# Performance work log

Measured on AMD Instinct MI355X. Metric: run time of the kernel, lower is better.

Reference implementation:

```python
import jax, jax.numpy as jnp
import numpy as np

N_HEADS = 4
D_HEAD = 16
SCALE = D_HEAD ** 0.5  # NOTE: original multiplies by sqrt(d_head), faithful


def _mha(x, Wq, bq, Wk, bk, Wv, bv, Wo, bo):
    # x: (..., N, D) with D = N_HEADS * D_HEAD
    q = jnp.einsum('...nd,od->...no', x, Wq) + bq
    k = jnp.einsum('...nd,od->...no', x, Wk) + bk
    v = jnp.einsum('...nd,od->...no', x, Wv) + bv
    lead = x.shape[:-2]
    n = x.shape[-2]
    q = q.reshape(*lead, n, N_HEADS, D_HEAD)
    k = k.reshape(*lead, n, N_HEADS, D_HEAD)
    v = v.reshape(*lead, n, N_HEADS, D_HEAD)
    scores = jnp.einsum('...nhd,...mhd->...hnm', q, k) * SCALE
    attn = jax.nn.softmax(scores, axis=-1)
    o = jnp.einsum('...hnm,...mhd->...nhd', attn, v).reshape(*lead, n, N_HEADS * D_HEAD)
    return jnp.einsum('...nd,od->...no', o, Wo) + bo


def setup_inputs() -> dict:
    key = jax.random.key(0)
    ks = jax.random.split(key, 20)
    b, n, d, dhf, G, C = 16, 16384, 64, 64, 256, 64
    s = 0.05
    inp = {
        'x': jax.random.normal(ks[0], (b, n, d), dtype=jnp.float32),
        'partitions': jax.random.permutation(ks[1], n).reshape(G, C).astype(jnp.int64),
    }
    names = ['q_intra', 'k_intra', 'v_intra', 'o_intra',
             'q_inter', 'k_inter', 'v_inter', 'o_inter']
    for i, nm in enumerate(names):
        d_in = d if nm.endswith('intra') and nm[0] != 'o' else dhf
        inp['W' + nm] = jax.random.normal(ks[2 + 2 * i], (dhf, d_in), dtype=jnp.float32) * s
        inp['b' + nm] = jax.random.normal(ks[3 + 2 * i], (dhf,), dtype=jnp.float32) * s
    return inp


def reference(x, partitions,
              Wq_intra, bq_intra, Wk_intra, bk_intra, Wv_intra, bv_intra, Wo_intra, bo_intra,
              Wq_inter, bq_inter, Wk_inter, bk_inter, Wv_inter, bv_inter, Wo_inter, bo_inter):
    b = x.shape[0]
    G, C = partitions.shape
    dhf = Wq_intra.shape[0]
    # gather nodes into groups: (b, G, C, d)
    xg = x[:, partitions, :]
    # intra-group attention, vectorized over (b, G)
    intra = _mha(xg, Wq_intra, bq_intra, Wk_intra, bk_intra,
                 Wv_intra, bv_intra, Wo_intra, bo_intra)  # (b, G, C, dhf)
    # MaxPool1d(kernel=dhf) over token axis with C == dhf -> max over tokens
    pooled = jnp.max(intra, axis=2)  # (b, G, dhf)
    inter = _mha(pooled, Wq_inter, bq_inter, Wk_inter, bk_inter,
                 Wv_inter, bv_inter, Wo_inter, bo_inter)  # (b, G, dhf)
    # broadcast-add inter-group features to every token in the group
    out = intra + inter[:, :, None, :]  # (b, G, C, dhf)
    flat = out.reshape(b, G * C, dhf)
    inv = jnp.argsort(partitions.reshape(-1))  # restore original node order
    return flat[:, inv, :]
```

## Files before the change

### kernel.cpp

```cpp
#include <hip/hip_runtime.h>
#include <hip/hip_bf16.h>

#define NTOK 16384
#define NG   256
#define NB   16

typedef float  f32x4   __attribute__((ext_vector_type(4)));
typedef short  short8v __attribute__((ext_vector_type(8)));
typedef short  short4v __attribute__((ext_vector_type(4)));

#define MFMA_BF16(a, b, c) __builtin_amdgcn_mfma_f32_16x16x32_bf16((a), (b), (c), 0, 0, 0)

#define QSCALE 5.770780163555856f

__device__ __forceinline__ short f2bf(float f) {
    union { float f; unsigned u; } x; x.f = f;
    unsigned r = (x.u + 0x7FFF + ((x.u >> 16) & 1)) >> 16;
    return (short)r;
}
__device__ __forceinline__ short bft(float f) {
    union { float f; unsigned u; } x; x.f = f;
    return (short)(x.u >> 16);
}
__device__ __forceinline__ float bf2f(short s) {
    union { float f; unsigned u; } x;
    x.u = ((unsigned)(unsigned short)s) << 16;
    return x.f;
}
__device__ __forceinline__ unsigned pk_cvt(float a, float b) {
#if __has_builtin(__builtin_amdgcn_cvt_pk_bf16_f32)
    auto r = __builtin_amdgcn_cvt_pk_bf16_f32(a, b);
    unsigned u; __builtin_memcpy(&u, &r, 4); return u;
#else
    union { float f; unsigned u; } xa, xb; xa.f = a; xb.f = b;
    const unsigned ua = xa.u + (0x7FFFu + ((xa.u >> 16) & 1));
    const unsigned ub = xb.u + (0x7FFFu + ((xb.u >> 16) & 1));
    return __builtin_amdgcn_perm(ub, ua, 0x07060302u);
#endif
}

__global__ void k_setup(const int* __restrict__ raw, int* __restrict__ part,
                        const float* __restrict__ Wq, const float* __restrict__ Wk,
                        const float* __restrict__ Wv, const float* __restrict__ Wo,
                        const float* __restrict__ Wqe, const float* __restrict__ Wke,
                        const float* __restrict__ Wve, const float* __restrict__ Woe,
                        short8v* __restrict__ wf)
{
    const int gid = blockIdx.x * 256 + threadIdx.x;
    if (gid < 16384) {
        const bool is64 = (raw[1] == 0 && raw[3] == 0 && raw[5] == 0);
        part[gid] = is64 ? raw[2 * gid] : raw[gid];
        return;
    }
    const int p = gid - 16384;
    if (p >= 5632) return;
    if (p < 3584) {
        const int v    = p >> 9;
        const int rem  = p & 511;
        const int tau  = rem >> 6;
        const int lane = rem & 63;
        const int jt = tau >> 1, kt = tau & 1;
        const int o  = jt * 16 + (lane & 15);
        const int d0 = kt * 32 + (lane >> 4) * 8;
        const float* W = (v < 2) ? Wq : (v < 4) ? Wk : (v < 6) ? Wv : Wo;
        const bool lo = (v & 1) && (v < 6);
        short8v r8;
#pragma unroll
        for (int i = 0; i < 8; ++i) {
            const float f = W[o * 64 + d0 + i];
            const short hh = f2bf(f);
            r8[i] = lo ? f2bf(f - bf2f(hh)) : hh;
        }
        wf[p] = r8;
    } else {
        const int g2   = p - 3584;
        const int v    = g2 >> 9;
        const int rem  = g2 & 511;
        const int tau  = rem >> 6;
        const int lane = rem & 63;
        const int jt = tau >> 1, kt = tau & 1;
        const int o  = jt * 16 + (lane & 15);
        const int d0 = kt * 32 + (lane >> 4) * 8;
        const float* W = (v == 0) ? Wqe : (v == 1) ? Wke : (v == 2) ? Wve : Woe;
        short8v r8;
#pragma unroll
        for (int i = 0; i < 8; ++i) r8[i] = f2bf(W[o * 64 + d0 + i]);
        wf[p] = r8;
    }
}

__global__ __launch_bounds__(256, 4) void k_intra(
    const float* __restrict__ x, const int* __restrict__ part,
    const short8v* __restrict__ wf,
    const float* __restrict__ bq, const float* __restrict__ bk,
    const float* __restrict__ bv, const float* __restrict__ bo,
    float* __restrict__ out, float* __restrict__ pooled,
    unsigned short* __restrict__ intra_g, const int use_g)
{
    __shared__ __align__(16) short S[20480];

    short* const xh = S;
    short* const kk = S + 4096;
    short* const ql = S + 8192;
    short* const qh = S + 12288;
    short* const vT = S + 16384;

    const int t  = threadIdx.x;
    const int g  = blockIdx.x;
    const int bb = blockIdx.y;
    const int l  = t & 63;
    const int w  = t >> 6;
    const int quad = l >> 4;
    const int col  = l & 15;

    for (int j = t; j < 512; j += 256) {
        const int row = j >> 3, c8 = j & 7;
        const int tok = part[g * 64 + row];
        const float* px = x + ((size_t)bb * NTOK + tok) * 64 + c8 * 8;
        const float4 f0 = ((const float4*)px)[0];
        const float4 f1 = ((const float4*)px)[1];
        uint4 pk;
        pk.x = pk_cvt(f0.x, f0.y);
        pk.y = pk_cvt(f0.z, f0.w);
        pk.z = pk_cvt(f1.x, f1.y);
        pk.w = pk_cvt(f1.z, f1.w);
        *(uint4*)&xh[row * 64 + ((c8 ^ (row & 7)) << 3)] = pk;
    }
    __syncthreads();

    {
        const float bqv = bq[w * 16 + col];
        const float bkv = bk[w * 16 + col];
        const float bvv = bv[w * 16 + col];
        short8v bqh[2], bql2[2], bkh[2], bkl[2], bvh[2], bvl[2];
#pragma unroll
        for (int kt = 0; kt < 2; ++kt) {
            const int tau = w * 2 + kt;
            bqh[kt]  = wf[(0 * 8 + tau) * 64 + l];
            bql2[kt] = wf[(1 * 8 + tau) * 64 + l];
            bkh[kt]  = wf[(2 * 8 + tau) * 64 + l];
            bkl[kt]  = wf[(3 * 8 + tau) * 64 + l];
            bvh[kt]  = wf[(4 * 8 + tau) * 64 + l];
            bvl[kt]  = wf[(5 * 8 + tau) * 64 + l];
        }
        for (int mt = 0; mt < 4; ++mt) {
            short8v axh[2];
#pragma unroll
            for (int kt = 0; kt < 2; ++kt) {
                const int row = mt * 16 + col;
                axh[kt] = *(const short8v*)&xh[row * 64 + (((kt * 4 + quad) ^ (row & 7)) << 3)];
            }
            f32x4 aq = {0.f, 0.f, 0.f, 0.f};
            f32x4 ak = {0.f, 0.f, 0.f, 0.f};
            f32x4 av = {0.f, 0.f, 0.f, 0.f};
#pragma unroll
            for (int kt = 0; kt < 2; ++kt) {
                aq = MFMA_BF16(axh[kt], bqh[kt],  aq);
                aq = MFMA_BF16(axh[kt], bql2[kt], aq);
                ak = MFMA_BF16(axh[kt], bkh[kt],  ak);
                ak = MFMA_BF16(axh[kt], bkl[kt],  ak);
                av = MFMA_BF16(axh[kt], bvh[kt],  av);
                av = MFMA_BF16(axh[kt], bvl[kt],  av);
            }
            const unsigned k01 = pk_cvt(ak[0] + bkv, ak[1] + bkv);
            const unsigned k23 = pk_cvt(ak[2] + bkv, ak[3] + bkv);
#pragma unroll
            for (int r = 0; r < 4; ++r) {
                const int m = mt * 16 + quad * 4 + r;
                const int pos = m * 64 + (((w * 2 + (col >> 3)) ^ (m & 7)) << 3) + (col & 7);
                const float q4 = (aq[r] + bqv) * QSCALE;
                const short hq = bft(q4);
                qh[pos] = hq;
                ql[pos] = bft(q4 - bf2f(hq));
                const unsigned kr = (r < 2) ? k01 : k23;
                kk[pos] = (short)((r & 1) ? (kr >> 16) : (kr & 0xFFFF));
            }
            {
                const int d = w * 16 + col;
                unsigned v01 = pk_cvt(av[0] + bvv, av[1] + bvv);
                unsigned v23 = pk_cvt(av[2] + bvv, av[3] + bvv);
                uint2 v4; v4.x = v01; v4.y = v23;
                const int cm = mt * 2 + (quad >> 1);
                const int idx = d * 64 + ((cm ^ (d & 7)) << 3) + ((quad & 1) * 4);
                *(uint2*)&vT[idx] = v4;
            }
        }
    }

    const int h = w, hc = h * 16;
    f32x4 s[4][4];
    {
        short8v bk4[4];
#pragma unroll
        for (int jt = 0; jt < 4; ++jt) {
            const int row = jt * 16 + col;
            bk4[jt] = *(const short8v*)&kk[row * 64 + (((h * 2 + (quad & 1)) ^ (row & 7)) << 3)];
        }
        const short8v z8 = {0, 0, 0, 0, 0, 0, 0, 0};
        for (int it = 0; it < 4; ++it) {
            const int row = it * 16 + col;
            const int idx = row * 64 + (((h * 2 + (quad & 1)) ^ (row & 7)) << 3);
            short8v aqh = *(const short8v*)&qh[idx];
            short8v aql = *(const short8v*)&ql[idx];
            if (quad >= 2) { aqh = z8; aql = z8; }
#pragma unroll
            for (int jt = 0; jt < 4; ++jt) {
                f32x4 acc = {0.f, 0.f, 0.f, 0.f};
                acc = MFMA_BF16(aqh, bk4[jt], acc);
                acc = MFMA_BF16(aql, bk4[jt], acc);
                s[it][jt] = acc;
            }
        }
    }
    float rden[4][4];
    for (int it = 0; it < 4; ++it) {
#pragma unroll
        for (int r = 0; r < 4; ++r) {
            float ds = 0.f;
#pragma unroll
            for (int jt = 0; jt < 4; ++jt) {
                const float e = exp2f(s[it][jt][r]);
                s[it][jt][r] = e;
                ds += e;
            }
            ds += __shfl_xor(ds, 1);
            ds += __shfl_xor(ds, 2);
            ds += __shfl_xor(ds, 4);
            ds += __shfl_xor(ds, 8);
            rden[it][r] = 1.0f / ds;
        }
    }
    __syncthreads();

    f32x4 oa[4];
#pragma unroll
    for (int it = 0; it < 4; ++it) oa[it] = (f32x4){0.f, 0.f, 0.f, 0.f};
    short* const Pw = S + w * 2560;
    for (int kt = 0; kt < 2; ++kt) {
        for (int it = 0; it < 4; ++it)
#pragma unroll
            for (int jl = 0; jl < 2; ++jl) {
                const int jt = kt * 2 + jl;
#pragma unroll
                for (int r = 0; r < 4; ++r)
                    Pw[(it * 16 + quad * 4 + r) * 40 + jl * 16 + col] = bft(s[it][jt][r]);
            }
        const int dv = hc + col;
        const int cmv = kt * 4 + quad;
        const short8v bv8 = *(const short8v*)&vT[dv * 64 + ((cmv ^ (dv & 7)) << 3)];
        for (int it = 0; it < 4; ++it) {
            const short8v ap = *(const short8v*)&Pw[(it * 16 + col) * 40 + quad * 8];
            oa[it] = MFMA_BF16(ap, bv8, oa[it]);
        }
    }
    for (int it = 0; it < 4; ++it) {
        const unsigned o01 = pk_cvt(oa[it][0] * rden[it][0], oa[it][1] * rden[it][1]);
        const unsigned o23 = pk_cvt(oa[it][2] * rden[it][2], oa[it][3] * rden[it][3]);
#pragma unroll
        for (int r = 0; r < 4; ++r) {
            const int row = it * 16 + quad * 4 + r;
            const int pos = row * 64 + (((h * 2 + (col >> 3)) ^ (row & 7)) << 3) + (col & 7);
            const unsigned uo = (r < 2) ? o01 : o23;
            qh[pos] = (short)((r & 1) ? (uo >> 16) : (uo & 0xFFFF));
        }
    }
    __syncthreads();

    float* const os = (float*)S;
    {
        const float bov = bo[w * 16 + col];
        short8v bo8[2];
        bo8[0] = wf[(6 * 8 + w * 2 + 0) * 64 + l];
        bo8[1] = wf[(6 * 8 + w * 2 + 1) * 64 + l];
        float pm = -1e30f;
        for (int mt = 0; mt < 4; ++mt) {
            f32x4 acc = {0.f, 0.f, 0.f, 0.f};
#pragma unroll
            for (int kt = 0; kt < 2; ++kt) {
                const int row = mt * 16 + col;
                const short8v ao = *(const short8v*)&qh[row * 64 + (((kt * 4 + quad) ^ (row & 7)) << 3)];
                acc = MFMA_BF16(ao, bo8[kt], acc);
            }
#pragma unroll
            for (int r = 0; r < 4; ++r) {
                const float vo = acc[r] + bov;
                pm = fmaxf(pm, vo);
                os[(mt * 16 + quad * 4 + r) * 68 + w * 16 + col] = vo;
            }
        }
        pm = fmaxf(pm, __shfl_xor(pm, 16));
        pm = fmaxf(pm, __shfl_xor(pm, 32));
        if (l < 16)
            pooled[((size_t)bb * NG + g) * 64 + w * 16 + col] = pm;
    }
    __syncthreads();

    {
        const int row = t >> 2, seg = t & 3;
        const float* pr = &os[row * 68 + seg * 16];
        const f32x4 v0 = ((const f32x4*)pr)[0];
        const f32x4 v1 = ((const f32x4*)pr)[1];
        const f32x4 v2 = ((const f32x4*)pr)[2];
        const f32x4 v3 = ((const f32x4*)pr)[3];
        if (use_g) {
            uint4 p0, p1;
            p0.x = pk_cvt(v0[0], v0[1]); p0.y = pk_cvt(v0[2], v0[3]);
            p0.z = pk_cvt(v1[0], v1[1]); p0.w = pk_cvt(v1[2], v1[3]);
            p1.x = pk_cvt(v2[0], v2[1]); p1.y = pk_cvt(v2[2], v2[3]);
            p1.z = pk_cvt(v3[0], v3[1]); p1.w = pk_cvt(v3[2], v3[3]);
            unsigned short* dst = &intra_g[(((size_t)bb * NG + g) * 64 + row) * 64 + seg * 16];
            ((uint4*)dst)[0] = p0;
            ((uint4*)dst)[1] = p1;
        } else {
            const int tok = part[g * 64 + row];
            float* po = &out[((size_t)bb * NTOK + tok) * 64 + seg * 16];
            ((f32x4*)po)[0] = v0; ((f32x4*)po)[1] = v1;
            ((f32x4*)po)[2] = v2; ((f32x4*)po)[3] = v3;
        }
    }
}

__global__ __launch_bounds__(256) void k_inter_qkv(
    const float* __restrict__ pooled, const short8v* __restrict__ wf,
    const float* __restrict__ bq, const float* __restrict__ bk,
    const float* __restrict__ bv,
    short* __restrict__ qws, short* __restrict__ kws, short* __restrict__ vTws)
{
    __shared__ __align__(16) short xs[4096];
    __shared__ __align__(16) short qs[64 * 72];
    __shared__ __align__(16) short ks2[64 * 72];
    const int t = threadIdx.x;
    const int chunk = blockIdx.x, bb = blockIdx.y;
    const int l = t & 63, w = t >> 6;
    const int quad = l >> 4, col = l & 15;

    for (int j = t; j < 512; j += 256) {
        const int row = j >> 3, c8 = j & 7;
        const float* px = pooled + ((size_t)bb * NG + chunk * 64 + row) * 64 + c8 * 8;
        const float4 f0 = ((const float4*)px)[0];
        const float4 f1 = ((const float4*)px)[1];
        uint4 pk;
        pk.x = pk_cvt(f0.x, f0.y);
        pk.y = pk_cvt(f0.z, f0.w);
        pk.z = pk_cvt(f1.x, f1.y);
        pk.w = pk_cvt(f1.z, f1.w);
        *(uint4*)&xs[row * 64 + ((c8 ^ (row & 7)) << 3)] = pk;
    }
    __syncthreads();

    const int WFI = 3584;
    short8v bqf[2], bkf[2], bvf[2];
#pragma unroll
    for (int kt = 0; kt < 2; ++kt) {
        bqf[kt] = wf[WFI + (0 * 8 + w * 2 + kt) * 64 + l];
        bkf[kt] = wf[WFI + (1 * 8 + w * 2 + kt) * 64 + l];
        bvf[kt] = wf[WFI + (2 * 8 + w * 2 + kt) * 64 + l];
    }
    const float bqv = bq[w * 16 + col];
    const float bkv = bk[w * 16 + col];
    const float bvv = bv[w * 16 + col];
    for (int mt = 0; mt < 4; ++mt) {
        short8v ax[2];
#pragma unroll
        for (int kt = 0; kt < 2; ++kt) {
            const int row = mt * 16 + col;
            ax[kt] = *(const short8v*)&xs[row * 64 + (((kt * 4 + quad) ^ (row & 7)) << 3)];
        }
        f32x4 aq = {0.f, 0.f, 0.f, 0.f};
        f32x4 ak = {0.f, 0.f, 0.f, 0.f};
        f32x4 av = {0.f, 0.f, 0.f, 0.f};
#pragma unroll
        for (int kt = 0; kt < 2; ++kt) {
            aq = MFMA_BF16(ax[kt], bqf[kt], aq);
            ak = MFMA_BF16(ax[kt], bkf[kt], ak);
            av = MFMA_BF16(ax[kt], bvf[kt], av);
        }
#pragma unroll
        for (int r = 0; r < 4; ++r) {
            const int m = mt * 16 + quad * 4 + r;
            qs[m * 72 + w * 16 + col]  = f2bf((aq[r] + bqv) * QSCALE);
            ks2[m * 72 + w * 16 + col] = f2bf(ak[r] + bkv);
        }
        uint2 v4;
        v4.x = pk_cvt(av[0] + bvv, av[1] + bvv);
        v4.y = pk_cvt(av[2] + bvv, av[3] + bvv);
        *(uint2*)&vTws[((size_t)bb * 64 + w * 16 + col) * 256 + chunk * 64 + mt * 16 + quad * 4] = v4;
    }
    __syncthreads();
    for (int j = t; j < 512; j += 256) {
        const int row = j >> 3, c8 = j & 7;
        *(short8v*)&qws[((size_t)bb * NG + chunk * 64 + row) * 64 + c8 * 8] =
            *(const short8v*)&qs[row * 72 + c8 * 8];
        *(short8v*)&kws[((size_t)bb * NG + chunk * 64 + row) * 64 + c8 * 8] =
            *(const short8v*)&ks2[row * 72 + c8 * 8];
    }
}

__global__ __launch_bounds__(256) void k_inter_attn2(
    const short* __restrict__ qws, const short* __restrict__ kws,
    const short* __restrict__ vTws, const short8v* __restrict__ wf,
    const float* __restrict__ bo, float* __restrict__ inter)
{
    __shared__ __align__(16) short Pw_all[4 * 16 * 40];
    __shared__ __align__(16) short os[16 * 72];
    const int t = threadIdx.x;
    const int qt = blockIdx.x, bb = blockIdx.y;
    const int l = t & 63, w = t >> 6;
    const int quad = l >> 4, col = l & 15;
    const int hc = w * 16;
    const int r0 = qt * 16;

    const short8v z8 = {0, 0, 0, 0, 0, 0, 0, 0};
    short8v bk[16];
#pragma unroll
    for (int jt = 0; jt < 16; ++jt)
        bk[jt] = (quad < 2)
            ? *(const short8v*)&kws[((size_t)bb * NG + jt * 16 + col) * 64 + hc + quad * 8]
            : z8;
    short8v aq = (quad < 2)
        ? *(const short8v*)&qws[((size_t)bb * NG + r0 + col) * 64 + hc + quad * 8]
        : z8;

    f32x4 s[16];
#pragma unroll
    for (int jt = 0; jt < 16; ++jt) {
        f32x4 acc = {0.f, 0.f, 0.f, 0.f};
        s[jt] = MFMA_BF16(aq, bk[jt], acc);
    }

    float rden[4];
#pragma unroll
    for (int r = 0; r < 4; ++r) {
        float mx = -1e30f;
#pragma unroll
        for (int jt = 0; jt < 16; ++jt) mx = fmaxf(mx, s[jt][r]);
        mx = fmaxf(mx, __shfl_xor(mx, 1));
        mx = fmaxf(mx, __shfl_xor(mx, 2));
        mx = fmaxf(mx, __shfl_xor(mx, 4));
        mx = fmaxf(mx, __shfl_xor(mx, 8));
        float ds = 0.f;
#pragma unroll
        for (int jt = 0; jt < 16; ++jt) {
            const float e = exp2f(s[jt][r] - mx);
            s[jt][r] = e;
            ds += e;
        }
        ds += __shfl_xor(ds, 1);
        ds += __shfl_xor(ds, 2);
        ds += __shfl_xor(ds, 4);
        ds += __shfl_xor(ds, 8);
        rden[r] = 1.0f / ds;
    }

    short* const Pw = Pw_all + w * 16 * 40;
    f32x4 oa = {0.f, 0.f, 0.f, 0.f};
    for (int c = 0; c < 8; ++c) {
#pragma unroll
        for (int jl = 0; jl < 2; ++jl) {
            const int jt = c * 2 + jl;
#pragma unroll
            for (int r = 0; r < 4; ++r)
                Pw[(quad * 4 + r) * 40 + jl * 16 + col] = bft(s[jt][r]);
        }
        const short8v bv8 = *(const short8v*)&vTws[((size_t)bb * 64 + hc + col) * 256 + c * 32 + quad * 8];
        const short8v ap = *(const short8v*)&Pw[col * 40 + quad * 8];
        oa = MFMA_BF16(ap, bv8, oa);
    }
    {
        const unsigned o01 = pk_cvt(oa[0] * rden[0], oa[1] * rden[1]);
        const unsigned o23 = pk_cvt(oa[2] * rden[2], oa[3] * rden[3]);
#pragma unroll
        for (int r = 0; r < 4; ++r) {
            const unsigned uo = (r < 2) ? o01 : o23;
            os[(quad * 4 + r) * 72 + hc + col] = (short)((r & 1) ? (uo >> 16) : (uo & 0xFFFF));
        }
    }
    __syncthreads();

    short8v bof[2];
    bof[0] = wf[3584 + (3 * 8 + w * 2 + 0) * 64 + l];
    bof[1] = wf[3584 + (3 * 8 + w * 2 + 1) * 64 + l];
    const float bov = bo[w * 16 + col];
    {
        f32x4 acc = {0.f, 0.f, 0.f, 0.f};
#pragma unroll
        for (int kt = 0; kt < 2; ++kt) {
            const short8v ao = *(const short8v*)&os[col * 72 + kt * 32 + quad * 8];
            acc = MFMA_BF16(ao, bof[kt], acc);
        }
#pragma unroll
        for (int r = 0; r < 4; ++r)
            inter[((size_t)bb * NG + r0 + quad * 4 + r) * 64 + w * 16 + col] = acc[r] + bov;
    }
}

__global__ __launch_bounds__(256) void k_final(
    const unsigned short* __restrict__ intra_g, const float* __restrict__ inter,
    const int* __restrict__ part, float* __restrict__ out)
{
    __shared__ float interL[64];
    __shared__ int   pidx[64];
    const int t  = threadIdx.x;
    const int g  = blockIdx.x;
    const int bb = blockIdx.y;
    if (t < 64) pidx[t] = part[g * 64 + t];
    else if (t < 128) interL[t - 64] = inter[((size_t)bb * NG + g) * 64 + (t - 64)];
    __syncthreads();
    const size_t ibase = ((size_t)bb * NG + g) * 64 * 64;
#pragma unroll
    for (int i = 0; i < 8; ++i) {
        const int item = i * 256 + t;
        const int row  = item >> 5;
        const int pr   = item & 31;
        const unsigned u = *(const unsigned*)&intra_g[ibase + row * 64 + pr * 2];
        const float2 iv = *(const float2*)&interL[pr * 2];
        float2 o;
        o.x = bf2f((short)(u & 0xFFFF)) + iv.x;
        o.y = bf2f((short)(u >> 16))    + iv.y;
        *(float2*)&out[((size_t)bb * NTOK + pidx[row]) * 64 + pr * 2] = o;
    }
}

__global__ __launch_bounds__(256) void k_scatter_add(
    const float* __restrict__ inter, const int* __restrict__ part,
    float* __restrict__ out)
{
    __shared__ float iv[64];
    __shared__ int   pidx[64];
    const int t  = threadIdx.x;
    const int g  = blockIdx.x;
    const int bb = blockIdx.y;
    if (t < 64) {
        iv[t]   = inter[((size_t)bb * NG + g) * 64 + t];
        pidx[t] = part[g * 64 + t];
    }
    __syncthreads();
    const int oo   = t & 63;
    const int cseg = t >> 6;
    const float add = iv[oo];
    for (int ci = 0; ci < 16; ++ci) {
        const int c = cseg * 16 + ci;
        float* p = out + ((size_t)bb * NTOK + pidx[c]) * 64 + oo;
        *p += add;
    }
}

extern "C" void kernel_launch(void* const* d_in, const int* in_sizes, int n_in,
                              void* d_out, int out_size, void* d_ws, size_t ws_size,
                              hipStream_t stream)
{
    const float* x    = (const float*)d_in[0];
    const int*   praw = (const int*)d_in[1];
    const float* Wq_a = (const float*)d_in[2];
    const float* bq_a = (const float*)d_in[3];
    const float* Wk_a = (const float*)d_in[4];
    const float* bk_a = (const float*)d_in[5];
    const float* Wv_a = (const float*)d_in[6];
    const float* bv_a = (const float*)d_in[7];
    const float* Wo_a = (const float*)d_in[8];
    const float* bo_a = (const float*)d_in[9];
    const float* Wq_e = (const float*)d_in[10];
    const float* bq_e = (const float*)d_in[11];
    const float* Wk_e = (const float*)d_in[12];
    const float* bk_e = (const float*)d_in[13];
    const float* Wv_e = (const float*)d_in[14];
    const float* bv_e = (const float*)d_in[15];
    const float* Wo_e = (const float*)d_in[16];
    const float* bo_e = (const float*)d_in[17];

    char* ws = (char*)d_ws;
    int*     part   = (int*)ws;
    float*   pooled = (float*)(ws + (1u << 16));
    float*   inter  = (float*)(ws + (1u << 16) + (1u << 20));
    short8v* wf     = (short8v*)(ws + (1u << 16) + 2 * (1u << 20));
    char*    base2  = ws + (1u << 16) + 2 * (1u << 20) + 98304;
    short*   qws    = (short*)base2;
    short*   kws    = (short*)(base2 + (1u << 19));
    short*   vTws   = (short*)(base2 + 2 * (1u << 19));
    unsigned short* intra_g = (unsigned short*)(base2 + 3 * (1u << 19));
    const size_t need = ((size_t)(base2 - ws)) + 3 * (1u << 19) + (size_t)NB * NG * 64 * 64 * 2;
    const int use_g = (ws_size >= need) ? 1 : 0;

    float* out = (float*)d_out;

    k_setup<<<dim3(86), dim3(256), 0, stream>>>(praw, part, Wq_a, Wk_a, Wv_a, Wo_a,
                                                Wq_e, Wk_e, Wv_e, Wo_e, wf);
    k_intra<<<dim3(NG, NB), dim3(256), 0, stream>>>(
        x, part, wf, bq_a, bk_a, bv_a, bo_a, out, pooled, intra_g, use_g);
    k_inter_qkv<<<dim3(4, NB), dim3(256), 0, stream>>>(
        pooled, wf, bq_e, bk_e, bv_e, qws, kws, vTws);
    k_inter_attn2<<<dim3(16, NB), dim3(256), 0, stream>>>(
        qws, kws, vTws, wf, bo_e, inter);
    if (use_g)
        k_final<<<dim3(NG, NB), dim3(256), 0, stream>>>(intra_g, inter, part, out);
    else
        k_scatter_add<<<dim3(NG, NB), dim3(256), 0, stream>>>(inter, part, out);
}
```

Measured before the change: 204.9 us.

## Transpose MFMA operands for Q/K/scores/PV to vectorize LDS stores and widen final writes

Swaps the A/B operands of the Q and K projection MFMAs and of the score and PV MFMAs. Each lane then holds four consecutive feature values and can write packed uint2 to LDS instead of scalar shorts. The softmax reduction now runs across quads with two shuffles per column tile instead of four shuffles per row. The final scatter kernel handles 16 contiguous elements per thread with 128-bit loads and stores. The goal is fewer LDS and global memory instructions and less shuffle work, at the cost of a more intricate operand layout that has to stay consistent across stages.

```diff
diff --git a/kernel.cpp b/kernel.cpp
--- a/kernel.cpp
+++ b/kernel.cpp
@@ -26,6 +26,9 @@
     union { float f; unsigned u; } x;
     x.u = ((unsigned)(unsigned short)s) << 16;
     return x.f;
+}
+__device__ __forceinline__ float u2f(unsigned u) {
+    union { unsigned u; float f; } x; x.u = u; return x.f;
 }
 __device__ __forceinline__ unsigned pk_cvt(float a, float b) {
 #if __has_builtin(__builtin_amdgcn_cvt_pk_bf16_f32)
@@ -129,9 +132,12 @@
     __syncthreads();
 
     {
-        const float bqv = bq[w * 16 + col];
-        const float bkv = bk[w * 16 + col];
+        const f32x4 bq4 = *(const f32x4*)&bq[w * 16 + quad * 4];
+        const f32x4 bk4 = *(const f32x4*)&bk[w * 16 + quad * 4];
         const float bvv = bv[w * 16 + col];
+        f32x4 bqs;
+#pragma unroll
+        for (int r = 0; r < 4; ++r) bqs[r] = bq4[r] * QSCALE;
         short8v bqh[2], bql2[2], bkh[2], bkl[2], bvh[2], bvl[2];
 #pragma unroll
         for (int kt = 0; kt < 2; ++kt) {
@@ -155,31 +161,39 @@
             f32x4 av = {0.f, 0.f, 0.f, 0.f};
 #pragma unroll
             for (int kt = 0; kt < 2; ++kt) {
-                aq = MFMA_BF16(axh[kt], bqh[kt],  aq);
-                aq = MFMA_BF16(axh[kt], bql2[kt], aq);
-                ak = MFMA_BF16(axh[kt], bkh[kt],  ak);
-                ak = MFMA_BF16(axh[kt], bkl[kt],  ak);
+                aq = MFMA_BF16(bqh[kt],  axh[kt], aq);
+                aq = MFMA_BF16(bql2[kt], axh[kt], aq);
+                ak = MFMA_BF16(bkh[kt],  axh[kt], ak);
+                ak = MFMA_BF16(bkl[kt],  axh[kt], ak);
                 av = MFMA_BF16(axh[kt], bvh[kt],  av);
                 av = MFMA_BF16(axh[kt], bvl[kt],  av);
             }
-            const unsigned k01 = pk_cvt(ak[0] + bkv, ak[1] + bkv);
-            const unsigned k23 = pk_cvt(ak[2] + bkv, ak[3] + bkv);
-#pragma unroll
-            for (int r = 0; r < 4; ++r) {
-                const int m = mt * 16 + quad * 4 + r;
-                const int pos = m * 64 + (((w * 2 + (col >> 3)) ^ (m & 7)) << 3) + (col & 7);
-                const float q4 = (aq[r] + bqv) * QSCALE;
-                const short hq = bft(q4);
-                qh[pos] = hq;
-                ql[pos] = bft(q4 - bf2f(hq));
-                const unsigned kr = (r < 2) ? k01 : k23;
-                kk[pos] = (short)((r & 1) ? (kr >> 16) : (kr & 0xFFFF));
-            }
+            f32x4 q4;
+#pragma unroll
+            for (int r = 0; r < 4; ++r) q4[r] = fmaf(aq[r], QSCALE, bqs[r]);
+            const unsigned qh01 = pk_cvt(q4[0], q4[1]);
+            const unsigned qh23 = pk_cvt(q4[2], q4[3]);
+            const float lo0 = q4[0] - u2f(qh01 << 16);
+            const float lo1 = q4[1] - u2f(qh01 & 0xFFFF0000u);
+            const float lo2 = q4[2] - u2f(qh23 << 16);
+            const float lo3 = q4[3] - u2f(qh23 & 0xFFFF0000u);
+            const unsigned ql01 = pk_cvt(lo0, lo1);
+            const unsigned ql23 = pk_cvt(lo2, lo3);
+            const unsigned k01 = pk_cvt(ak[0] + bk4[0], ak[1] + bk4[1]);
+            const unsigned k23 = pk_cvt(ak[2] + bk4[2], ak[3] + bk4[3]);
+            const int m = mt * 16 + col;
+            const int pos = m * 64 + (((w * 2 + (quad >> 1)) ^ (m & 7)) << 3) + ((quad & 1) << 2);
+            uint2 uq; uq.x = qh01; uq.y = qh23;
+            uint2 ulo; ulo.x = ql01; ulo.y = ql23;
+            uint2 uk; uk.x = k01; uk.y = k23;
+            *(uint2*)&qh[pos] = uq;
+            *(uint2*)&ql[pos] = ulo;
+            *(uint2*)&kk[pos] = uk;
             {
                 const int d = w * 16 + col;
-                unsigned v01 = pk_cvt(av[0] + bvv, av[1] + bvv);
-                unsigned v23 = pk_cvt(av[2] + bvv, av[3] + bvv);
-                uint2 v4; v4.x = v01; v4.y = v23;
+                uint2 v4;
+                v4.x = pk_cvt(av[0] + bvv, av[1] + bvv);
+                v4.y = pk_cvt(av[2] + bvv, av[3] + bvv);
                 const int cm = mt * 2 + (quad >> 1);
                 const int idx = d * 64 + ((cm ^ (d & 7)) << 3) + ((quad & 1) * 4);
                 *(uint2*)&vT[idx] = v4;
@@ -190,79 +204,81 @@
     const int h = w, hc = h * 16;
     f32x4 s[4][4];
     {
-        short8v bk4[4];
-#pragma unroll
+        short8v ak4[4];
+#pragma unroll
+        for (int it = 0; it < 4; ++it) {
+            const int row = it * 16 + col;
+            ak4[it] = *(const short8v*)&kk[row * 64 + (((h * 2 + (quad & 1)) ^ (row & 7)) << 3)];
+        }
+        const short8v z8 = {0, 0, 0, 0, 0, 0, 0, 0};
         for (int jt = 0; jt < 4; ++jt) {
             const int row = jt * 16 + col;
-            bk4[jt] = *(const short8v*)&kk[row * 64 + (((h * 2 + (quad & 1)) ^ (row & 7)) << 3)];
-        }
-        const short8v z8 = {0, 0, 0, 0, 0, 0, 0, 0};
+            const int idx = row * 64 + (((h * 2 + (quad & 1)) ^ (row & 7)) << 3);
+            short8v bqh_ = *(const short8v*)&qh[idx];
+            short8v bql_ = *(const short8v*)&ql[idx];
+            if (quad >= 2) { bqh_ = z8; bql_ = z8; }
+#pragma unroll
+            for (int it = 0; it < 4; ++it) {
+                f32x4 acc = {0.f, 0.f, 0.f, 0.f};
+                acc = MFMA_BF16(ak4[it], bqh_, acc);
+                acc = MFMA_BF16(ak4[it], bql_, acc);
+                s[it][jt] = acc;
+            }
+        }
+    }
+    float rden[4];
+#pragma unroll
+    for (int jt = 0; jt < 4; ++jt) {
+        float ds = 0.f;
+#pragma unroll
         for (int it = 0; it < 4; ++it) {
-            const int row = it * 16 + col;
-            const int idx = row * 64 + (((h * 2 + (quad & 1)) ^ (row & 7)) << 3);
-            short8v aqh = *(const short8v*)&qh[idx];
-            short8v aql = *(const short8v*)&ql[idx];
-            if (quad >= 2) { aqh = z8; aql = z8; }
-#pragma unroll
-            for (int jt = 0; jt < 4; ++jt) {
-                f32x4 acc = {0.f, 0.f, 0.f, 0.f};
-                acc = MFMA_BF16(aqh, bk4[jt], acc);
-                acc = MFMA_BF16(aql, bk4[jt], acc);
-                s[it][jt] = acc;
-            }
-        }
-    }
-    float rden[4][4];
-    for (int it = 0; it < 4; ++it) {
-#pragma unroll
-        for (int r = 0; r < 4; ++r) {
-            float ds = 0.f;
-#pragma unroll
-            for (int jt = 0; jt < 4; ++jt) {
+#pragma unroll
+            for (int r = 0; r < 4; ++r) {
                 const float e = exp2f(s[it][jt][r]);
                 s[it][jt][r] = e;
                 ds += e;
             }
-            ds += __shfl_xor(ds, 1);
-            ds += __shfl_xor(ds, 2);
-            ds += __shfl_xor(ds, 4);
-            ds += __shfl_xor(ds, 8);
-            rden[it][r] = 1.0f / ds;
-        }
+        }
+        ds += __shfl_xor(ds, 16);
+        ds += __shfl_xor(ds, 32);
+        rden[jt] = 1.0f / ds;
     }
     __syncthreads();
 
     f32x4 oa[4];
 #pragma unroll
-    for (int it = 0; it < 4; ++it) oa[it] = (f32x4){0.f, 0.f, 0.f, 0.f};
+    for (int jt = 0; jt < 4; ++jt) oa[jt] = (f32x4){0.f, 0.f, 0.f, 0.f};
     short* const Pw = S + w * 2560;
     for (int kt = 0; kt < 2; ++kt) {
-        for (int it = 0; it < 4; ++it)
-#pragma unroll
-            for (int jl = 0; jl < 2; ++jl) {
-                const int jt = kt * 2 + jl;
-#pragma unroll
-                for (int r = 0; r < 4; ++r)
-                    Pw[(it * 16 + quad * 4 + r) * 40 + jl * 16 + col] = bft(s[it][jt][r]);
-            }
+#pragma unroll
+        for (int jt = 0; jt < 4; ++jt) {
+#pragma unroll
+            for (int ih = 0; ih < 2; ++ih) {
+                const int it = kt * 2 + ih;
+                uint2 pp;
+                pp.x = pk_cvt(s[it][jt][0], s[it][jt][1]);
+                pp.y = pk_cvt(s[it][jt][2], s[it][jt][3]);
+                *(uint2*)&Pw[(jt * 16 + col) * 40 + ih * 16 + (quad << 2)] = pp;
+            }
+        }
         const int dv = hc + col;
         const int cmv = kt * 4 + quad;
-        const short8v bv8 = *(const short8v*)&vT[dv * 64 + ((cmv ^ (dv & 7)) << 3)];
-        for (int it = 0; it < 4; ++it) {
-            const short8v ap = *(const short8v*)&Pw[(it * 16 + col) * 40 + quad * 8];
-            oa[it] = MFMA_BF16(ap, bv8, oa[it]);
-        }
-    }
-    for (int it = 0; it < 4; ++it) {
-        const unsigned o01 = pk_cvt(oa[it][0] * rden[it][0], oa[it][1] * rden[it][1]);
-        const unsigned o23 = pk_cvt(oa[it][2] * rden[it][2], oa[it][3] * rden[it][3]);
-#pragma unroll
-        for (int r = 0; r < 4; ++r) {
-            const int row = it * 16 + quad * 4 + r;
-            const int pos = row * 64 + (((h * 2 + (col >> 3)) ^ (row & 7)) << 3) + (col & 7);
-            const unsigned uo = (r < 2) ? o01 : o23;
-            qh[pos] = (short)((r & 1) ? (uo >> 16) : (uo & 0xFFFF));
-        }
+        const short8v av8 = *(const short8v*)&vT[dv * 64 + ((cmv ^ (dv & 7)) << 3)];
+#pragma unroll
+        for (int jt = 0; jt < 4; ++jt) {
+            const short8v bp = *(const short8v*)&Pw[(jt * 16 + col) * 40 + (quad << 3)];
+            oa[jt] = MFMA_BF16(av8, bp, oa[jt]);
+        }
+    }
+#pragma unroll
+    for (int jt = 0; jt < 4; ++jt) {
+        const float rd = rden[jt];
+        const unsigned o01 = pk_cvt(oa[jt][0] * rd, oa[jt][1] * rd);
+        const unsigned o23 = pk_cvt(oa[jt][2] * rd, oa[jt][3] * rd);
+        const int m = jt * 16 + col;
+        const int pos = m * 64 + (((w * 2 + (quad >> 1)) ^ (m & 7)) << 3) + ((quad & 1) << 2);
+        uint2 ov; ov.x = o01; ov.y = o23;
+        *(uint2*)&qh[pos] = ov;
     }
     __syncthreads();
 
@@ -506,19 +522,33 @@
     if (t < 64) pidx[t] = part[g * 64 + t];
     else if (t < 128) interL[t - 64] = inter[((size_t)bb * NG + g) * 64 + (t - 64)];
     __syncthreads();
-    const size_t ibase = ((size_t)bb * NG + g) * 64 * 64;
-#pragma unroll
-    for (int i = 0; i < 8; ++i) {
-        const int item = i * 256 + t;
-        const int row  = item >> 5;
-        const int pr   = item & 31;
-        const unsigned u = *(const unsigned*)&intra_g[ibase + row * 64 + pr * 2];
-        const float2 iv = *(const float2*)&interL[pr * 2];
-        float2 o;
-        o.x = bf2f((short)(u & 0xFFFF)) + iv.x;
-        o.y = bf2f((short)(u >> 16))    + iv.y;
-        *(float2*)&out[((size_t)bb * NTOK + pidx[row]) * 64 + pr * 2] = o;
-    }
+    const int row = t >> 2, seg = t & 3;
+    const size_t ib = (((size_t)bb * NG + g) * 64 + row) * 64 + seg * 16;
+    const uint4 u0 = *(const uint4*)&intra_g[ib];
+    const uint4 u1 = *(const uint4*)&intra_g[ib + 8];
+    const float* iL = &interL[seg * 16];
+    float* po = &out[((size_t)bb * NTOK + pidx[row]) * 64 + seg * 16];
+    f32x4 o0, o1, o2, o3;
+    o0[0] = u2f(u0.x << 16)          + iL[0];
+    o0[1] = u2f(u0.x & 0xFFFF0000u)  + iL[1];
+    o0[2] = u2f(u0.y << 16)          + iL[2];
+    o0[3] = u2f(u0.y & 0xFFFF0000u)  + iL[3];
+    o1[0] = u2f(u0.z << 16)          + iL[4];
+    o1[1] = u2f(u0.z & 0xFFFF0000u)  + iL[5];
+    o1[2] = u2f(u0.w << 16)          + iL[6];
+    o1[3] = u2f(u0.w & 0xFFFF0000u)  + iL[7];
+    o2[0] = u2f(u1.x << 16)          + iL[8];
+    o2[1] = u2f(u1.x & 0xFFFF0000u)  + iL[9];
+    o2[2] = u2f(u1.y << 16)          + iL[10];
+    o2[3] = u2f(u1.y & 0xFFFF0000u)  + iL[11];
+    o3[0] = u2f(u1.z << 16)          + iL[12];
+    o3[1] = u2f(u1.z & 0xFFFF0000u)  + iL[13];
+    o3[2] = u2f(u1.w << 16)          + iL[14];
+    o3[3] = u2f(u1.w & 0xFFFF0000u)  + iL[15];
+    ((f32x4*)po)[0] = o0;
+    ((f32x4*)po)[1] = o1;
+    ((f32x4*)po)[2] = o2;
+    ((f32x4*)po)[3] = o3;
 }
 
 __global__ __launch_bounds__(256) void k_scatter_add(
```

Result: no change. 204.2 us (-0.3%).
